# Kernel tuning notes

Measured on AMD Instinct MI355X. Metric: run time of the kernel, lower is better.

The kernel has to match this reference:

```python
import jax, jax.numpy as jnp
import numpy as np

NQ = 23          # number of qubits -> statevector dim 2**23
NC = 23          # circuit width used by config_circuit_fun
NUM_BLOCK = 1    # number of repeated blocks


def _config_circuit(nc, nq, num_block):
    # UID 0 = parametrized single-qubit gate, UID 1 = CNOT
    uid_block = [0] * nc + [1] * (nc - 1)
    qid_block = list(range(nc))
    for q in range(nc - 1):
        # qubitID_fun(q0=q, q1=q+1, Nq) = q*(Nq-1) + (q+1-q-1) % Nq = q*(Nq-1)
        qid_block.append(q * (nq - 1))
    return uid_block * num_block, qid_block * num_block


def _u3(theta):
    # General single-qubit gate U = Rz(a) @ Ry(b) @ Rz(c), theta = (a, b, c)
    a = theta[0].astype(jnp.complex64)
    c = theta[2].astype(jnp.complex64)
    cb = jnp.cos(theta[1] * 0.5).astype(jnp.complex64)
    sb = jnp.sin(theta[1] * 0.5).astype(jnp.complex64)
    ea, eA = jnp.exp(-0.5j * a), jnp.exp(0.5j * a)
    ec, eC = jnp.exp(-0.5j * c), jnp.exp(0.5j * c)
    row0 = jnp.stack([ea * cb * ec, -ea * sb * eC])
    row1 = jnp.stack([eA * sb * ec, eA * cb * eC])
    return jnp.stack([row0, row1])  # (2, 2) complex64


def _apply1(U, q, state):
    # apply 2x2 gate U on qubit q of statevector (length 2**NQ)
    st = state.reshape(2 ** q, 2, -1)
    return jnp.einsum('ij,ajb->aib', U, st).reshape(-1)


def _apply2(U4, q0, q1, state):
    # apply 4x4 gate on qubits (q0, q1), q0 < q1
    st = state.reshape(2 ** q0, 2, 2 ** (q1 - q0 - 1), 2, -1)
    Ut = U4.reshape(2, 2, 2, 2)  # (out0, out1, in0, in1)
    return jnp.einsum('ijkl,akblc->aibjc', Ut, st).reshape(-1)


def setup_inputs() -> dict:
    key = jax.random.key(0)
    k1, k2, k3 = jax.random.split(key, 3)
    depth = (2 * NC - 1) * NUM_BLOCK
    param = jax.random.normal(k1, (depth * 3,), dtype=jnp.float32)
    re = jax.random.normal(k2, (2 ** NQ,), dtype=jnp.float32)
    im = jax.random.normal(k3, (2 ** NQ,), dtype=jnp.float32)
    nrm = jnp.sqrt(jnp.sum(re * re + im * im))
    return {"state_re": re / nrm, "state_im": im / nrm, "param": param}


def reference(state_re, state_im, param):
    uids, qids = _config_circuit(NC, NQ, NUM_BLOCK)
    depth = len(uids)
    th = param.reshape(depth, 3)
    cnot = jnp.array([[1, 0, 0, 0],
                      [0, 1, 0, 0],
                      [0, 0, 0, 1],
                      [0, 0, 1, 0]], dtype=jnp.complex64)
    state = (state_re + 1j * state_im).astype(jnp.complex64)
    for i in range(depth):
        if uids[i] == 0:
            state = _apply1(_u3(th[i]), qids[i], state)
        else:
            q0 = qids[i] // (NQ - 1)
            q1 = (qids[i] - q0 * (NQ - 1) + q0 + 1) % NQ
            state = _apply2(cnot, q0, q1, state)
    # return real/imag stacked (schema has no complex dtype)
    return jnp.stack([jnp.real(state), jnp.imag(state)])
```

## Files before the change

kernel.cpp:

```cpp
#include <hip/hip_runtime.h>
#include <math.h>


#define NTOT (1u << 23)

struct G8 { float r00,i00,r01,i01,r10,i10,r11,i11; };

__device__ __forceinline__ G8 u3_lane(const float* __restrict__ p, int q) {
    float a = p[3*q+0], b = p[3*q+1], c = p[3*q+2];
    float cb = cosf(b*0.5f), sb = sinf(b*0.5f);
    float ph = (a+c)*0.5f, m = (a-c)*0.5f;
    float cp = cosf(ph), sp = sinf(ph);
    float cm = cosf(m),  sm = sinf(m);
    G8 g;
    g.r00 =  cb*cp; g.i00 = -cb*sp;
    g.r01 = -sb*cm; g.i01 =  sb*sm;
    g.r10 =  sb*cm; g.i10 =  sb*sm;
    g.r11 =  cb*cp; g.i11 =  cb*sp;
    return g;
}

__device__ __forceinline__ G8 bc(const G8& m, int q) {
    G8 g;
    g.r00 = __shfl(m.r00, q); g.i00 = __shfl(m.i00, q);
    g.r01 = __shfl(m.r01, q); g.i01 = __shfl(m.i01, q);
    g.r10 = __shfl(m.r10, q); g.i10 = __shfl(m.i10, q);
    g.r11 = __shfl(m.r11, q); g.i11 = __shfl(m.i11, q);
    return g;
}

__device__ __forceinline__ void bfs(float& x0r, float& x0i, float& x1r, float& x1i, const G8& g) {
    float y0r = g.r00*x0r - g.i00*x0i + g.r01*x1r - g.i01*x1i;
    float y0i = g.r00*x0i + g.i00*x0r + g.r01*x1i + g.i01*x1r;
    float y1r = g.r10*x0r - g.i10*x0i + g.r11*x1r - g.i11*x1i;
    float y1i = g.r10*x0i + g.i10*x0r + g.r11*x1i + g.i11*x1r;
    x0r=y0r; x0i=y0i; x1r=y1r; x1i=y1i;
}

__device__ __forceinline__ void bf4v(float4& ar, float4& ai, float4& br, float4& bi, const G8& g) {
    bfs(ar.x, ai.x, br.x, bi.x, g);
    bfs(ar.y, ai.y, br.y, bi.y, g);
    bfs(ar.z, ai.z, br.z, bi.z, g);
    bfs(ar.w, ai.w, br.w, bi.w, g);
}

__device__ __forceinline__ void bfc0(float4& r, float4& i, const G8& g) {
    bfs(r.x, i.x, r.y, i.y, g); bfs(r.z, i.z, r.w, i.w, g);
}
__device__ __forceinline__ void bfc1(float4& r, float4& i, const G8& g) {
    bfs(r.x, i.x, r.z, i.z, g); bfs(r.y, i.y, r.w, i.w, g);
}

__device__ __forceinline__ void reg_gate0(float4 (&xr)[4], float4 (&xi)[4], const G8& g) {
    bf4v(xr[0],xi[0],xr[1],xi[1],g); bf4v(xr[2],xi[2],xr[3],xi[3],g);
}
__device__ __forceinline__ void reg_gate1(float4 (&xr)[4], float4 (&xi)[4], const G8& g) {
    bf4v(xr[0],xi[0],xr[2],xi[2],g); bf4v(xr[1],xi[1],xr[3],xi[3],g);
}

__device__ __forceinline__ float4 sx4(float4 v, int m) {
    float4 r;
    r.x = __shfl_xor(v.x, m); r.y = __shfl_xor(v.y, m);
    r.z = __shfl_xor(v.z, m); r.w = __shfl_xor(v.w, m);
    return r;
}

__device__ __forceinline__ void lane_gate(float4 (&xr)[4], float4 (&xi)[4], const G8& g, int bit, int m) {
    float cor = bit ? g.r11 : g.r00, coi = bit ? g.i11 : g.i00;
    float cpr = bit ? g.r10 : g.r01, cpi = bit ? g.i10 : g.i01;
#pragma unroll
    for (int i = 0; i < 4; ++i) {
        float4 pr = sx4(xr[i], m), pi = sx4(xi[i], m);
        float4 nr, ni;
        nr.x = cor*xr[i].x - coi*xi[i].x + cpr*pr.x - cpi*pi.x;
        ni.x = cor*xi[i].x + coi*xr[i].x + cpr*pi.x + cpi*pr.x;
        nr.y = cor*xr[i].y - coi*xi[i].y + cpr*pr.y - cpi*pi.y;
        ni.y = cor*xi[i].y + coi*xr[i].y + cpr*pi.y + cpi*pr.y;
        nr.z = cor*xr[i].z - coi*xi[i].z + cpr*pr.z - cpi*pi.z;
        ni.z = cor*xi[i].z + coi*xr[i].z + cpr*pi.z + cpi*pr.z;
        nr.w = cor*xr[i].w - coi*xi[i].w + cpr*pr.w - cpi*pi.w;
        ni.w = cor*xi[i].w + coi*xr[i].w + cpr*pi.w + cpi*pr.w;
        xr[i] = nr; xi[i] = ni;
    }
}

__device__ __forceinline__ int swz(int q) { return q ^ ((q>>3)&7) ^ ((q>>6)&7); }
__device__ __forceinline__ int la(int p)  { return ((p>>4)<<9) | ((p&15)<<4); }

__device__ __forceinline__ int pxor12(int x) { x^=x>>1; x^=x>>2; x^=x>>4; x^=x>>8; return x & 0xFFF; }
__device__ __forceinline__ int pxor9(int x)  { x^=x>>1; x^=x>>2; x^=x>>4; x^=x>>8; return x & 0x1FF; }

__global__ __launch_bounds__(1024)
void pass_high(const float* __restrict__ in_re, const float* __restrict__ in_im,
               const float* __restrict__ param,
               float* __restrict__ out_re, float* __restrict__ out_im) {
    __shared__ __align__(16) char L[131072];
    const int tid = threadIdx.x, blk = blockIdx.x;
    const int l = tid & 63, w = tid >> 6;
    G8 my = u3_lane(param, l < 23 ? l : 22);
    float4 xr[4], xi[4];

    const float4* R4 = (const float4*)in_re;
    const float4* I4 = (const float4*)in_im;
    const int rbase = ((l>>3)<<2) | (w<<5);
    const size_t gb0 = ((size_t)blk << 3) | (size_t)(l & 7);
#pragma unroll
    for (int j = 0; j < 4; ++j) {
        size_t gi = (((size_t)(rbase | j)) << 12) | gb0;
        xr[j] = R4[gi]; xi[j] = I4[gi];
    }
    { G8 g = bc(my,22);
#pragma unroll
      for (int j = 0; j < 4; ++j) bfc0(xr[j], xi[j], g); }
    { G8 g = bc(my,21);
#pragma unroll
      for (int j = 0; j < 4; ++j) bfc1(xr[j], xi[j], g); }
    { G8 g = bc(my,8); reg_gate0(xr, xi, g); }
    { G8 g = bc(my,7); reg_gate1(xr, xi, g); }
    { G8 g = bc(my,6); lane_gate(xr, xi, g, (l>>3)&1,  8); }
    { G8 g = bc(my,5); lane_gate(xr, xi, g, (l>>4)&1, 16); }
    { G8 g = bc(my,4); lane_gate(xr, xi, g, (l>>5)&1, 32); }
#pragma unroll
    for (int j = 0; j < 4; ++j) {
        int a = la(swz((l & 7) | (j << 3) | ((l >> 3) << 5) | (w << 8)));
        *(float4*)(L + a) = xr[j];
        *(float4*)(L + a + 256) = xi[j];
    }
    __syncthreads();
    const int qb = ((l >> 2) & 15) | (w << 4) | ((l & 3) << 10);
#pragma unroll
    for (int j = 0; j < 4; ++j) {
        int a = la(swz(qb | (j << 8)));
        xr[j] = *(const float4*)(L + a);
        xi[j] = *(const float4*)(L + a + 256);
    }
    { G8 g = bc(my,3); reg_gate0(xr, xi, g); }
    { G8 g = bc(my,2); reg_gate1(xr, xi, g); }
    { G8 g = bc(my,1); lane_gate(xr, xi, g, (l>>0)&1, 1); }
    { G8 g = bc(my,0); lane_gate(xr, xi, g, (l>>1)&1, 2); }
    float4* OR4 = (float4*)out_re;
    float4* OI4 = (float4*)out_im;
    const int row_base = ((l >> 5) & 1) | (w << 1) | ((l & 3) << 7);
    const int sb = pxor9(row_base);
    const size_t ob0 = ((size_t)blk << 3) | (size_t)((l >> 2) & 7);
    constexpr int SM[4] = {0, 0x3F, 0x7F, 0x40};
#pragma unroll
    for (int j = 0; j < 4; ++j) {
        size_t oi = (((size_t)(sb ^ SM[j])) << 12) | ob0;
        OR4[oi] = xr[j]; OI4[oi] = xi[j];
    }
}

__global__ __launch_bounds__(1024)
void pass_low(float* __restrict__ sre, float* __restrict__ sim,
              const float* __restrict__ param) {
    __shared__ __align__(16) char L[131072];
    const int tid = threadIdx.x, c = blockIdx.x;
    const int l = tid & 63, w = tid >> 6;
    G8 my = u3_lane(param, l < 23 ? l : 22);
    float4 xr[4], xi[4];

    float4* R4 = (float4*)sre;
    float4* I4 = (float4*)sim;
    const size_t gb = ((size_t)c << 12) | (size_t)(l | (w << 8));
#pragma unroll
    for (int j = 0; j < 4; ++j) {
        xr[j] = R4[gb + (size_t)(j << 6)];
        xi[j] = I4[gb + (size_t)(j << 6)];
    }
    { G8 g = bc(my,20); lane_gate(xr, xi, g, (l>>0)&1,  1); }
    { G8 g = bc(my,19); lane_gate(xr, xi, g, (l>>1)&1,  2); }
    { G8 g = bc(my,18); lane_gate(xr, xi, g, (l>>2)&1,  4); }
    { G8 g = bc(my,17); lane_gate(xr, xi, g, (l>>3)&1,  8); }
    { G8 g = bc(my,16); lane_gate(xr, xi, g, (l>>4)&1, 16); }
    { G8 g = bc(my,15); lane_gate(xr, xi, g, (l>>5)&1, 32); }
    { G8 g = bc(my,14); reg_gate0(xr, xi, g); }
    { G8 g = bc(my,13); reg_gate1(xr, xi, g); }
#pragma unroll
    for (int j = 0; j < 4; ++j) {
        int a = la(swz(l | (j << 6) | (w << 8)));
        *(float4*)(L + a) = xr[j];
        *(float4*)(L + a + 256) = xi[j];
    }
    __syncthreads();
    const int qb = ((l >> 2) & 15) | (w << 4) | ((l & 3) << 10);
#pragma unroll
    for (int j = 0; j < 4; ++j) {
        int a = la(swz(qb | (j << 8)));
        xr[j] = *(const float4*)(L + a);
        xi[j] = *(const float4*)(L + a + 256);
    }
    { G8 g = bc(my,12); reg_gate0(xr, xi, g); }
    { G8 g = bc(my,11); reg_gate1(xr, xi, g); }
    { G8 g = bc(my,10); lane_gate(xr, xi, g, (l>>0)&1, 1); }
    { G8 g = bc(my, 9); lane_gate(xr, xi, g, (l>>1)&1, 2); }
    const int px0 = pxor12(qb);
    const int codd = c & 1;
    const int A12 = codd ? 0xFFF : 0;
    constexpr int PM[4] = {0, 0x1FF, 0x3FF, 0x200};
#pragma unroll
    for (int j = 0; j < 4; ++j) {
        int pxj = px0 ^ PM[j];
        int of4 = pxj ^ A12;
        int b = (pxj ^ codd) & 1;
        float s0r = xr[j].x, s1r = xr[j].y, s2r = xr[j].w, s3r = xr[j].z;
        float s0i = xi[j].x, s1i = xi[j].y, s2i = xi[j].w, s3i = xi[j].z;
        float o0r = b ? s3r : s0r, o1r = b ? s2r : s1r, o2r = b ? s1r : s2r, o3r = b ? s0r : s3r;
        float o0i = b ? s3i : s0i, o1i = b ? s2i : s1i, o2i = b ? s1i : s2i, o3i = b ? s0i : s3i;
        size_t oo = ((size_t)c << 12) | (size_t)of4;
        R4[oo] = make_float4(o0r, o1r, o2r, o3r);
        I4[oo] = make_float4(o0i, o1i, o2i, o3i);
    }
}

extern "C" void kernel_launch(void* const* d_in, const int* in_sizes, int n_in,
                              void* d_out, int out_size, void* d_ws, size_t ws_size,
                              hipStream_t stream) {
    (void)in_sizes; (void)n_in; (void)d_ws; (void)ws_size; (void)out_size;
    const float* in_re = (const float*)d_in[0];
    const float* in_im = (const float*)d_in[1];
    const float* param = (const float*)d_in[2];
    float* out_re = (float*)d_out;
    float* out_im = (float*)d_out + NTOT;

    pass_high<<<512, 1024, 0, stream>>>(in_re, in_im, param, out_re, out_im);
    pass_low <<<512, 1024, 0, stream>>>(out_re, out_im, param);
}
```

Before: 88.27 us.

## Replace shuffle-based lane gates with DPP/permlane swaps and remap qubit layout

Gate matrices are now broadcast with readlane instead of shuffles, and cross-lane butterfly partners are fetched with DPP quad permutes and permlane16/32 swap builtins (where available) instead of ds_bpermute shuffles. The qubit-to-lane/register/LDS mapping in both passes is reworked so that lane-level gates use only the xor-1, xor-2, xor-16 and xor-32 distances those primitives support. LDS staging becomes unswizzled, with separate real and imaginary halves. This aims to cut LDS-routed shuffle traffic and latency, at the risk of LDS bank conflicts from the dropped swizzle. The fallback path for the xor-16 swap uses ds_swizzle, whose semantics may differ.

New measurement: 77.14 us. -12.6%, faster.

```diff
diff --git a/kernel.cpp b/kernel.cpp
--- a/kernel.cpp
+++ b/kernel.cpp
@@ -3,6 +3,8 @@
 
 
 #define NTOT (1u << 23)
+
+typedef unsigned int u2 __attribute__((ext_vector_type(2)));
 
 struct G8 { float r00,i00,r01,i01,r10,i10,r11,i11; };
 
@@ -20,12 +22,15 @@
     return g;
 }
 
-__device__ __forceinline__ G8 bc(const G8& m, int q) {
+__device__ __forceinline__ float rdl(float v, int q) {
+    return __uint_as_float(__builtin_amdgcn_readlane(__float_as_uint(v), q));
+}
+__device__ __forceinline__ G8 gread(const G8& m, int q) {
     G8 g;
-    g.r00 = __shfl(m.r00, q); g.i00 = __shfl(m.i00, q);
-    g.r01 = __shfl(m.r01, q); g.i01 = __shfl(m.i01, q);
-    g.r10 = __shfl(m.r10, q); g.i10 = __shfl(m.i10, q);
-    g.r11 = __shfl(m.r11, q); g.i11 = __shfl(m.i11, q);
+    g.r00=rdl(m.r00,q); g.i00=rdl(m.i00,q);
+    g.r01=rdl(m.r01,q); g.i01=rdl(m.i01,q);
+    g.r10=rdl(m.r10,q); g.i10=rdl(m.i10,q);
+    g.r11=rdl(m.r11,q); g.i11=rdl(m.i11,q);
     return g;
 }
 
@@ -36,21 +41,18 @@
     float y1i = g.r10*x0i + g.i10*x0r + g.r11*x1i + g.i11*x1r;
     x0r=y0r; x0i=y0i; x1r=y1r; x1i=y1i;
 }
-
 __device__ __forceinline__ void bf4v(float4& ar, float4& ai, float4& br, float4& bi, const G8& g) {
     bfs(ar.x, ai.x, br.x, bi.x, g);
     bfs(ar.y, ai.y, br.y, bi.y, g);
     bfs(ar.z, ai.z, br.z, bi.z, g);
     bfs(ar.w, ai.w, br.w, bi.w, g);
 }
-
 __device__ __forceinline__ void bfc0(float4& r, float4& i, const G8& g) {
     bfs(r.x, i.x, r.y, i.y, g); bfs(r.z, i.z, r.w, i.w, g);
 }
 __device__ __forceinline__ void bfc1(float4& r, float4& i, const G8& g) {
     bfs(r.x, i.x, r.z, i.z, g); bfs(r.y, i.y, r.w, i.w, g);
 }
-
 __device__ __forceinline__ void reg_gate0(float4 (&xr)[4], float4 (&xi)[4], const G8& g) {
     bf4v(xr[0],xi[0],xr[1],xi[1],g); bf4v(xr[2],xi[2],xr[3],xi[3],g);
 }
@@ -58,34 +60,75 @@
     bf4v(xr[0],xi[0],xr[2],xi[2],g); bf4v(xr[1],xi[1],xr[3],xi[3],g);
 }
 
-__device__ __forceinline__ float4 sx4(float4 v, int m) {
-    float4 r;
-    r.x = __shfl_xor(v.x, m); r.y = __shfl_xor(v.y, m);
-    r.z = __shfl_xor(v.z, m); r.w = __shfl_xor(v.w, m);
-    return r;
-}
-
-__device__ __forceinline__ void lane_gate(float4 (&xr)[4], float4 (&xi)[4], const G8& g, int bit, int m) {
+__device__ __forceinline__ float p_dpp1(float x) {
+    return __uint_as_float((unsigned)__builtin_amdgcn_update_dpp(
+        0, (int)__float_as_uint(x), 0xB1, 0xF, 0xF, true));
+}
+__device__ __forceinline__ float p_dpp2(float x) {
+    return __uint_as_float((unsigned)__builtin_amdgcn_update_dpp(
+        0, (int)__float_as_uint(x), 0x4E, 0xF, 0xF, true));
+}
+__device__ __forceinline__ float p_x16(float x, int hi) {
+#if __has_builtin(__builtin_amdgcn_permlane16_swap)
+    u2 r = __builtin_amdgcn_permlane16_swap(__float_as_uint(x), __float_as_uint(x), false, false);
+    return __uint_as_float(hi ? r[0] : r[1]);
+#else
+    (void)hi;
+    return __uint_as_float((unsigned)__builtin_amdgcn_ds_swizzle(
+        (int)__float_as_uint(x), 0x401F));
+#endif
+}
+__device__ __forceinline__ float p_x32(float x, int hi) {
+#if __has_builtin(__builtin_amdgcn_permlane32_swap)
+    u2 r = __builtin_amdgcn_permlane32_swap(__float_as_uint(x), __float_as_uint(x), false, false);
+    return __uint_as_float(hi ? r[0] : r[1]);
+#else
+    (void)hi;
+    return __shfl_xor(x, 32, 64);
+#endif
+}
+
+__device__ __forceinline__ void pcomb(float4 (&xr)[4], float4 (&xi)[4],
+                                      const float4 (&pr)[4], const float4 (&pi)[4],
+                                      const G8& g, int bit) {
     float cor = bit ? g.r11 : g.r00, coi = bit ? g.i11 : g.i00;
     float cpr = bit ? g.r10 : g.r01, cpi = bit ? g.i10 : g.i01;
 #pragma unroll
     for (int i = 0; i < 4; ++i) {
-        float4 pr = sx4(xr[i], m), pi = sx4(xi[i], m);
         float4 nr, ni;
-        nr.x = cor*xr[i].x - coi*xi[i].x + cpr*pr.x - cpi*pi.x;
-        ni.x = cor*xi[i].x + coi*xr[i].x + cpr*pi.x + cpi*pr.x;
-        nr.y = cor*xr[i].y - coi*xi[i].y + cpr*pr.y - cpi*pi.y;
-        ni.y = cor*xi[i].y + coi*xr[i].y + cpr*pi.y + cpi*pr.y;
-        nr.z = cor*xr[i].z - coi*xi[i].z + cpr*pr.z - cpi*pi.z;
-        ni.z = cor*xi[i].z + coi*xr[i].z + cpr*pi.z + cpi*pr.z;
-        nr.w = cor*xr[i].w - coi*xi[i].w + cpr*pr.w - cpi*pi.w;
-        ni.w = cor*xi[i].w + coi*xr[i].w + cpr*pi.w + cpi*pr.w;
+        nr.x = cor*xr[i].x - coi*xi[i].x + cpr*pr[i].x - cpi*pi[i].x;
+        ni.x = cor*xi[i].x + coi*xr[i].x + cpr*pi[i].x + cpi*pr[i].x;
+        nr.y = cor*xr[i].y - coi*xi[i].y + cpr*pr[i].y - cpi*pi[i].y;
+        ni.y = cor*xi[i].y + coi*xr[i].y + cpr*pi[i].y + cpi*pr[i].y;
+        nr.z = cor*xr[i].z - coi*xi[i].z + cpr*pr[i].z - cpi*pi[i].z;
+        ni.z = cor*xi[i].z + coi*xr[i].z + cpr*pi[i].z + cpi*pr[i].z;
+        nr.w = cor*xr[i].w - coi*xi[i].w + cpr*pr[i].w - cpi*pi[i].w;
+        ni.w = cor*xi[i].w + coi*xr[i].w + cpr*pi[i].w + cpi*pr[i].w;
         xr[i] = nr; xi[i] = ni;
     }
 }
 
-__device__ __forceinline__ int swz(int q) { return q ^ ((q>>3)&7) ^ ((q>>6)&7); }
-__device__ __forceinline__ int la(int p)  { return ((p>>4)<<9) | ((p&15)<<4); }
+#define MAKE_PGATE(NAME, FETCH)                                                     \
+__device__ __forceinline__ void NAME(float4 (&xr)[4], float4 (&xi)[4],              \
+                                     const G8& g, int bit, int hi) {                \
+    float4 pr[4], pi[4];                                                            \
+    _Pragma("unroll")                                                               \
+    for (int i = 0; i < 4; ++i) {                                                   \
+        pr[i].x = FETCH(xr[i].x); pr[i].y = FETCH(xr[i].y);                         \
+        pr[i].z = FETCH(xr[i].z); pr[i].w = FETCH(xr[i].w);                         \
+        pi[i].x = FETCH(xi[i].x); pi[i].y = FETCH(xi[i].y);                         \
+        pi[i].z = FETCH(xi[i].z); pi[i].w = FETCH(xi[i].w);                         \
+    }                                                                               \
+    (void)hi; pcomb(xr, xi, pr, pi, g, bit);                                        \
+}
+#define F_DPP1(v) p_dpp1(v)
+#define F_DPP2(v) p_dpp2(v)
+#define F_X16(v)  p_x16(v, hi)
+#define F_X32(v)  p_x32(v, hi)
+MAKE_PGATE(gate_dpp1, F_DPP1)
+MAKE_PGATE(gate_dpp2, F_DPP2)
+MAKE_PGATE(gate_x16,  F_X16)
+MAKE_PGATE(gate_x32,  F_X32)
 
 __device__ __forceinline__ int pxor12(int x) { x^=x>>1; x^=x>>2; x^=x>>4; x^=x>>8; return x & 0xFFF; }
 __device__ __forceinline__ int pxor9(int x)  { x^=x>>1; x^=x>>2; x^=x>>4; x^=x>>8; return x & 0x1FF; }
@@ -100,54 +143,62 @@
     G8 my = u3_lane(param, l < 23 ? l : 22);
     float4 xr[4], xi[4];
 
-    const float4* R4 = (const float4*)in_re;
-    const float4* I4 = (const float4*)in_im;
-    const int rbase = ((l>>3)<<2) | (w<<5);
+    const float4* R4p = (const float4*)in_re;
+    const float4* I4p = (const float4*)in_im;
+    const int rb = (l >> 3) | (w << 5);
     const size_t gb0 = ((size_t)blk << 3) | (size_t)(l & 7);
 #pragma unroll
     for (int j = 0; j < 4; ++j) {
-        size_t gi = (((size_t)(rbase | j)) << 12) | gb0;
-        xr[j] = R4[gi]; xi[j] = I4[gi];
-    }
-    { G8 g = bc(my,22);
+        size_t gi = (((size_t)(rb | (j << 3))) << 12) | gb0;
+        xr[j] = R4p[gi]; xi[j] = I4p[gi];
+    }
+    const int b1  = l & 1;
+    const int h16 = (l >> 4) & 1, h32 = (l >> 5) & 1;
+
+    { G8 g = gread(my,22);
 #pragma unroll
       for (int j = 0; j < 4; ++j) bfc0(xr[j], xi[j], g); }
-    { G8 g = bc(my,21);
+    { G8 g = gread(my,21);
 #pragma unroll
       for (int j = 0; j < 4; ++j) bfc1(xr[j], xi[j], g); }
-    { G8 g = bc(my,8); reg_gate0(xr, xi, g); }
-    { G8 g = bc(my,7); reg_gate1(xr, xi, g); }
-    { G8 g = bc(my,6); lane_gate(xr, xi, g, (l>>3)&1,  8); }
-    { G8 g = bc(my,5); lane_gate(xr, xi, g, (l>>4)&1, 16); }
-    { G8 g = bc(my,4); lane_gate(xr, xi, g, (l>>5)&1, 32); }
-#pragma unroll
-    for (int j = 0; j < 4; ++j) {
-        int a = la(swz((l & 7) | (j << 3) | ((l >> 3) << 5) | (w << 8)));
+    { G8 g = gread(my,5); reg_gate0(xr, xi, g); }
+    { G8 g = gread(my,4); reg_gate1(xr, xi, g); }
+    { G8 g = gread(my,7); gate_x16(xr, xi, g, h16, h16); }
+    { G8 g = gread(my,6); gate_x32(xr, xi, g, h32, h32); }
+
+#pragma unroll
+    for (int j = 0; j < 4; ++j) {
+        int a = ((w << 8) | (j << 6) | l) << 4;
         *(float4*)(L + a) = xr[j];
-        *(float4*)(L + a + 256) = xi[j];
+        *(float4*)(L + a + 65536) = xi[j];
     }
     __syncthreads();
-    const int qb = ((l >> 2) & 15) | (w << 4) | ((l & 3) << 10);
-#pragma unroll
-    for (int j = 0; j < 4; ++j) {
-        int a = la(swz(qb | (j << 8)));
+    const int sbase = ((l >> 1) & 7) | ((w & 3) << 4) | (((w >> 2) & 3) << 6)
+                    | (((l >> 4) & 3) << 9) | ((l & 1) << 11);
+    constexpr int OFF[4] = {0, 8, 256, 264};
+#pragma unroll
+    for (int j = 0; j < 4; ++j) {
+        int a = (sbase | OFF[j]) << 4;
         xr[j] = *(const float4*)(L + a);
-        xi[j] = *(const float4*)(L + a + 256);
-    }
-    { G8 g = bc(my,3); reg_gate0(xr, xi, g); }
-    { G8 g = bc(my,2); reg_gate1(xr, xi, g); }
-    { G8 g = bc(my,1); lane_gate(xr, xi, g, (l>>0)&1, 1); }
-    { G8 g = bc(my,0); lane_gate(xr, xi, g, (l>>1)&1, 2); }
+        xi[j] = *(const float4*)(L + a + 65536);
+    }
+
+    { G8 g = gread(my,8); reg_gate0(xr, xi, g); }
+    { G8 g = gread(my,3); reg_gate1(xr, xi, g); }
+    { G8 g = gread(my,0); gate_dpp1(xr, xi, g, b1, 0); }
+    { G8 g = gread(my,2); gate_x16(xr, xi, g, h16, h16); }
+    { G8 g = gread(my,1); gate_x32(xr, xi, g, h32, h32); }
+
     float4* OR4 = (float4*)out_re;
     float4* OI4 = (float4*)out_im;
-    const int row_base = ((l >> 5) & 1) | (w << 1) | ((l & 3) << 7);
-    const int sb = pxor9(row_base);
-    const size_t ob0 = ((size_t)blk << 3) | (size_t)((l >> 2) & 7);
-    constexpr int SM[4] = {0, 0x3F, 0x7F, 0x40};
-#pragma unroll
-    for (int j = 0; j < 4; ++j) {
-        size_t oi = (((size_t)(sb ^ SM[j])) << 12) | ob0;
-        OR4[oi] = xr[j]; OI4[oi] = xi[j];
+    const int row_base = ((w & 15) << 1) | (((l >> 4) & 3) << 6) | ((l & 1) << 8);
+    const int sg = pxor9(row_base);
+    const size_t ob = ((size_t)blk << 3) | (size_t)((l >> 1) & 7);
+    constexpr int SJ[4] = {0, 0x01, 0x3F, 0x3E};
+#pragma unroll
+    for (int j = 0; j < 4; ++j) {
+        size_t F = (((size_t)(sg ^ SJ[j])) << 12) | ob;
+        OR4[F] = xr[j]; OI4[F] = xi[j];
     }
 }
 
@@ -160,41 +211,48 @@
     G8 my = u3_lane(param, l < 23 ? l : 22);
     float4 xr[4], xi[4];
 
-    float4* R4 = (float4*)sre;
-    float4* I4 = (float4*)sim;
-    const size_t gb = ((size_t)c << 12) | (size_t)(l | (w << 8));
-#pragma unroll
-    for (int j = 0; j < 4; ++j) {
-        xr[j] = R4[gb + (size_t)(j << 6)];
-        xi[j] = I4[gb + (size_t)(j << 6)];
-    }
-    { G8 g = bc(my,20); lane_gate(xr, xi, g, (l>>0)&1,  1); }
-    { G8 g = bc(my,19); lane_gate(xr, xi, g, (l>>1)&1,  2); }
-    { G8 g = bc(my,18); lane_gate(xr, xi, g, (l>>2)&1,  4); }
-    { G8 g = bc(my,17); lane_gate(xr, xi, g, (l>>3)&1,  8); }
-    { G8 g = bc(my,16); lane_gate(xr, xi, g, (l>>4)&1, 16); }
-    { G8 g = bc(my,15); lane_gate(xr, xi, g, (l>>5)&1, 32); }
-    { G8 g = bc(my,14); reg_gate0(xr, xi, g); }
-    { G8 g = bc(my,13); reg_gate1(xr, xi, g); }
-#pragma unroll
-    for (int j = 0; j < 4; ++j) {
-        int a = la(swz(l | (j << 6) | (w << 8)));
+    float4* R4p = (float4*)sre;
+    float4* I4p = (float4*)sim;
+    const size_t cb = ((size_t)c) << 12;
+    const int sw0 = (w << 8) | l;
+#pragma unroll
+    for (int j = 0; j < 4; ++j) {
+        size_t fi = cb + (size_t)(sw0 | (j << 6));
+        xr[j] = R4p[fi]; xi[j] = I4p[fi];
+    }
+    const int b1 = l & 1, b2 = (l >> 1) & 1;
+    const int h16 = (l >> 4) & 1, h32 = (l >> 5) & 1;
+
+    { G8 g = gread(my,20); gate_dpp1(xr, xi, g, b1, 0); }
+    { G8 g = gread(my,19); gate_dpp2(xr, xi, g, b2, 0); }
+    { G8 g = gread(my,16); gate_x16(xr, xi, g, h16, h16); }
+    { G8 g = gread(my,15); gate_x32(xr, xi, g, h32, h32); }
+    { G8 g = gread(my,14); reg_gate0(xr, xi, g); }
+    { G8 g = gread(my,13); reg_gate1(xr, xi, g); }
+
+#pragma unroll
+    for (int j = 0; j < 4; ++j) {
+        int a = (sw0 | (j << 6)) << 4;
         *(float4*)(L + a) = xr[j];
-        *(float4*)(L + a + 256) = xi[j];
+        *(float4*)(L + a + 65536) = xi[j];
     }
     __syncthreads();
-    const int qb = ((l >> 2) & 15) | (w << 4) | ((l & 3) << 10);
-#pragma unroll
-    for (int j = 0; j < 4; ++j) {
-        int a = la(swz(qb | (j << 8)));
+    const int sbase = ((l >> 2) & 3) | ((l & 3) << 2) | ((w & 15) << 4) | (((l >> 4) & 3) << 10);
+#pragma unroll
+    for (int j = 0; j < 4; ++j) {
+        int a = (sbase | (j << 8)) << 4;
         xr[j] = *(const float4*)(L + a);
-        xi[j] = *(const float4*)(L + a + 256);
-    }
-    { G8 g = bc(my,12); reg_gate0(xr, xi, g); }
-    { G8 g = bc(my,11); reg_gate1(xr, xi, g); }
-    { G8 g = bc(my,10); lane_gate(xr, xi, g, (l>>0)&1, 1); }
-    { G8 g = bc(my, 9); lane_gate(xr, xi, g, (l>>1)&1, 2); }
-    const int px0 = pxor12(qb);
+        xi[j] = *(const float4*)(L + a + 65536);
+    }
+
+    { G8 g = gread(my,18); gate_dpp1(xr, xi, g, b1, 0); }
+    { G8 g = gread(my,17); gate_dpp2(xr, xi, g, b2, 0); }
+    { G8 g = gread(my,12); reg_gate0(xr, xi, g); }
+    { G8 g = gread(my,11); reg_gate1(xr, xi, g); }
+    { G8 g = gread(my,10); gate_x16(xr, xi, g, h16, h16); }
+    { G8 g = gread(my, 9); gate_x32(xr, xi, g, h32, h32); }
+
+    const int px0 = pxor12(sbase);
     const int codd = c & 1;
     const int A12 = codd ? 0xFFF : 0;
     constexpr int PM[4] = {0, 0x1FF, 0x3FF, 0x200};
@@ -207,9 +265,9 @@
         float s0i = xi[j].x, s1i = xi[j].y, s2i = xi[j].w, s3i = xi[j].z;
         float o0r = b ? s3r : s0r, o1r = b ? s2r : s1r, o2r = b ? s1r : s2r, o3r = b ? s0r : s3r;
         float o0i = b ? s3i : s0i, o1i = b ? s2i : s1i, o2i = b ? s1i : s2i, o3i = b ? s0i : s3i;
-        size_t oo = ((size_t)c << 12) | (size_t)of4;
-        R4[oo] = make_float4(o0r, o1r, o2r, o3r);
-        I4[oo] = make_float4(o0i, o1i, o2i, o3i);
+        size_t oo = cb | (size_t)of4;
+        R4p[oo] = make_float4(o0r, o1r, o2r, o3r);
+        I4p[oo] = make_float4(o0i, o1i, o2i, o3i);
     }
 }
 
```
